# Kernel optimization log

Hardware: AMD Instinct MI355X
Metric: run time of the kernel (lower is better)

The kernel has to match this reference:

```python
import jax, jax.numpy as jnp
import numpy as np

MARGIN = 0.3


def setup_inputs() -> dict:
    key = jax.random.key(0)
    k1, k2 = jax.random.split(key)
    B, D, N_IDS = 8192, 256, 512
    emb = jax.random.normal(k1, (B, D), dtype=jnp.float32)
    emb = emb / jnp.linalg.norm(emb, axis=1, keepdims=True)  # L2-normalized as docstring states
    labels = jax.random.randint(k2, (B,), 0, N_IDS, dtype=jnp.int64)
    return {"embeddings": emb, "labels": labels}


def reference(embeddings, labels):
    B = embeddings.shape[0]
    # pairwise Euclidean distance via cosine similarity (embeddings are L2-normalized)
    sim = jnp.matmul(embeddings, embeddings.T)              # (B, B)
    dist = jnp.sqrt(jnp.clip(2.0 - 2.0 * sim, 0.0) + 1e-12)
    same = labels[:, None] == labels[None, :]               # (B, B)
    eye = jnp.eye(B, dtype=bool)
    pos_mask = same & ~eye
    neg_mask = ~same
    neg_inf = jnp.asarray(-jnp.inf, dist.dtype)
    pos_inf = jnp.asarray(jnp.inf, dist.dtype)
    dist_ap = jnp.max(jnp.where(pos_mask, dist, neg_inf), axis=1)  # hardest positive per anchor
    dist_an = jnp.min(jnp.where(neg_mask, dist, pos_inf), axis=1)  # hardest negative per anchor
    valid = jnp.any(pos_mask, axis=1) & jnp.any(neg_mask, axis=1)
    # MarginRankingLoss(dist_an, dist_ap, y=1) = mean(relu(dist_ap - dist_an + margin)) over valid anchors
    per = jnp.maximum(dist_ap - dist_an + MARGIN, 0.0)
    per = jnp.where(valid, per, 0.0)
    n_valid = jnp.sum(valid.astype(dist.dtype))
    loss = jnp.where(n_valid > 0, jnp.sum(per) / jnp.maximum(n_valid, 1.0), 0.0)
    return loss
```

## Files before the change

### kernel.cpp

```cpp
#include <hip/hip_runtime.h>
#include <hip/hip_bf16.h>


#define BDIM 8192
#define DDIM 256

typedef short bf16x8 __attribute__((ext_vector_type(8)));
typedef float f32x4  __attribute__((ext_vector_type(4)));
typedef unsigned short u16;

static __device__ __forceinline__ bf16x8 ld_frag(const u16* p) {
    return *reinterpret_cast<const bf16x8*>(p);
}

static __device__ __forceinline__ u16 f2bf(float f) {
    union { float f; unsigned int u; } x; x.f = f;
    unsigned int u = x.u;
    unsigned int r = u + 0x7fffu + ((u >> 16) & 1u);
    return (u16)(r >> 16);
}

static __device__ __forceinline__ void gload_lds16(const u16* g, u16* l) {
    __builtin_amdgcn_global_load_lds(
        (const __attribute__((address_space(1))) unsigned int*)g,
        (__attribute__((address_space(3))) unsigned int*)l, 16, 0, 0);
}

__global__ __launch_bounds__(256) void cvt_init_kernel(const float* __restrict__ in,
                                                       u16* __restrict__ out,
                                                       int* __restrict__ minpos,
                                                       int* __restrict__ maxneg) {
    int i = blockIdx.x * 256 + threadIdx.x;
    const float4 v = reinterpret_cast<const float4*>(in)[i];
    ushort4 o;
    o.x = f2bf(v.x); o.y = f2bf(v.y); o.z = f2bf(v.z); o.w = f2bf(v.w);
    reinterpret_cast<ushort4*>(out)[i] = o;
    if (i < BDIM) {
        minpos[i] = 0x7f800000;
        maxneg[i] = 0;
    }
}

__global__ __launch_bounds__(256, 2) void triplet_main(const u16* __restrict__ Ebf,
                                                       const int* __restrict__ labels,
                                                       int* __restrict__ minpos,
                                                       int* __restrict__ maxneg) {
    __shared__ __align__(16) u16 smem[3][32 * DDIM];
    __shared__ int slab[256];
    __shared__ int colmin[256], colmax[256];

    const int tid  = threadIdx.x;
    const int w    = tid >> 6;
    const int l    = tid & 63;
    const int quad = l >> 4;
    const int r16  = l & 15;

    int t = blockIdx.x, bi = 0;
    while (t >= 32 - bi) { t -= 32 - bi; ++bi; }
    const int bu = bi + t;

    const int mblk  = bi * 256 + w * 64;
    const int nbase = bu * 256;

    slab[tid]   = labels[nbase + tid];
    colmin[tid] = 0x7f800000;
    colmax[tid] = 0;

    bf16x8 a[4][8];
#pragma unroll
    for (int ms = 0; ms < 4; ++ms) {
        const u16* ap = Ebf + (size_t)(mblk + ms * 16 + r16) * DDIM + quad * 8;
#pragma unroll
        for (int k = 0; k < 8; ++k) a[ms][k] = ld_frag(ap + k * 32);
    }

    int lab_row[4][4];
#pragma unroll
    for (int ms = 0; ms < 4; ++ms)
#pragma unroll
        for (int r = 0; r < 4; ++r)
            lab_row[ms][r] = labels[mblk + ms * 16 + quad * 4 + r];

    float minp[4][4], maxn[4][4];
#pragma unroll
    for (int ms = 0; ms < 4; ++ms)
#pragma unroll
        for (int r = 0; r < 4; ++r) { minp[ms][r] = __builtin_inff(); maxn[ms][r] = -__builtin_inff(); }

    const int qs = quad ^ (r16 & 3);
    const int s4 = (r16 >> 2) & 1;

    auto stage = [&](int tt, int buf) {
        const int n1 = nbase + tt * 32;
#pragma unroll
        for (int it = 0; it < 4; ++it) {
            const int q = it * 256 + tid;
            const int r = q >> 5;
            const int c = (q & 31) ^ (r & 7);
            gload_lds16(Ebf + ((size_t)(n1 + r) << 8) + c * 8,
                        &smem[buf][0] + it * 2048 + w * 512);
        }
    };

    stage(0, 0);
    stage(1, 1);

    int cur = 0;
#pragma unroll 1
    for (int nn = 0; nn < 8; ++nn) {
        if (nn < 7) asm volatile("s_waitcnt vmcnt(4) lgkmcnt(0)" ::: "memory");
        else        asm volatile("s_waitcnt vmcnt(0) lgkmcnt(0)" ::: "memory");
        __builtin_amdgcn_s_barrier();
        __builtin_amdgcn_sched_barrier(0);

        if (nn + 2 < 8) {
            const int stg = (cur >= 1) ? cur - 1 : 2;
            stage(nn + 2, stg);
        }

        const int n0 = nbase + nn * 32;

        if (n0 + 32 > mblk) {
            int lab_c[2];
            lab_c[0] = slab[nn * 32 + r16];
            lab_c[1] = slab[nn * 32 + 16 + r16];

            f32x4 acc[4][2];
#pragma unroll
            for (int ms = 0; ms < 4; ++ms)
#pragma unroll
                for (int nt = 0; nt < 2; ++nt)
                    acc[ms][nt] = (f32x4){0.f, 0.f, 0.f, 0.f};

            const u16* bb = &smem[cur][0];
            const u16* bnt[2];
#pragma unroll
            for (int nt = 0; nt < 2; ++nt)
                bnt[nt] = bb + (nt * 16 + r16) * DDIM + qs * 8;

            __builtin_amdgcn_s_setprio(1);
#pragma unroll
            for (int k = 0; k < 8; ++k) {
                const int koff = ((k ^ s4) << 5);
                bf16x8 b[2];
#pragma unroll
                for (int nt = 0; nt < 2; ++nt) b[nt] = ld_frag(bnt[nt] + koff);
#pragma unroll
                for (int ms = 0; ms < 4; ++ms)
#pragma unroll
                    for (int nt = 0; nt < 2; ++nt)
                        acc[ms][nt] = __builtin_amdgcn_mfma_f32_16x16x32_bf16(
                            a[ms][k], b[nt], acc[ms][nt], 0, 0, 0);
            }
            __builtin_amdgcn_s_setprio(0);

            float cmin[2], cmax[2];
#pragma unroll
            for (int nt = 0; nt < 2; ++nt) { cmin[nt] = __builtin_inff(); cmax[nt] = -__builtin_inff(); }

            const bool diagTile = (n0 < mblk + 64) && (mblk < n0 + 32);
            if (__builtin_expect(diagTile, 0)) {
#pragma unroll
                for (int nt = 0; nt < 2; ++nt) {
                    const int colg = n0 + nt * 16 + r16;
#pragma unroll
                    for (int ms = 0; ms < 4; ++ms)
#pragma unroll
                        for (int r = 0; r < 4; ++r) {
                            const int rowg = mblk + ms * 16 + quad * 4 + r;
                            const float s = acc[ms][nt][r];
                            const bool same = (lab_c[nt] == lab_row[ms][r]);
                            const bool pos  = same && (colg != rowg);
                            const float pv = pos  ?  s : __builtin_inff();
                            const float nv = same ? -__builtin_inff() : s;
                            minp[ms][r] = fminf(minp[ms][r], pv);
                            maxn[ms][r] = fmaxf(maxn[ms][r], nv);
                            cmin[nt] = fminf(cmin[nt], pv);
                            cmax[nt] = fmaxf(cmax[nt], nv);
                        }
                }
            } else {
#pragma unroll
                for (int nt = 0; nt < 2; ++nt)
#pragma unroll
                    for (int ms = 0; ms < 4; ++ms)
#pragma unroll
                        for (int r = 0; r < 4; ++r) {
                            const float s = acc[ms][nt][r];
                            const bool same = (lab_c[nt] == lab_row[ms][r]);
                            const float pv = same ?  s : __builtin_inff();
                            const float nv = same ? -__builtin_inff() : s;
                            minp[ms][r] = fminf(minp[ms][r], pv);
                            maxn[ms][r] = fmaxf(maxn[ms][r], nv);
                            cmin[nt] = fminf(cmin[nt], pv);
                            cmax[nt] = fmaxf(cmax[nt], nv);
                        }
            }

#pragma unroll
            for (int mask = 16; mask <= 32; mask <<= 1) {
#pragma unroll
                for (int nt = 0; nt < 2; ++nt) {
                    cmin[nt] = fminf(cmin[nt], __shfl_xor(cmin[nt], mask, 64));
                    cmax[nt] = fmaxf(cmax[nt], __shfl_xor(cmax[nt], mask, 64));
                }
            }
            if (quad == 0) {
#pragma unroll
                for (int nt = 0; nt < 2; ++nt) {
                    const int cl = nn * 32 + nt * 16 + r16;
                    atomicMin(&colmin[cl], __float_as_int(cmin[nt] + 2.0f));
                    atomicMax(&colmax[cl], __float_as_int(cmax[nt] + 2.0f));
                }
            }
        }

        cur = (cur == 2) ? 0 : cur + 1;
    }

#pragma unroll
    for (int mask = 1; mask <= 8; mask <<= 1) {
#pragma unroll
        for (int ms = 0; ms < 4; ++ms)
#pragma unroll
            for (int r = 0; r < 4; ++r) {
                minp[ms][r] = fminf(minp[ms][r], __shfl_xor(minp[ms][r], mask, 64));
                maxn[ms][r] = fmaxf(maxn[ms][r], __shfl_xor(maxn[ms][r], mask, 64));
            }
    }
    if (r16 == 0) {
#pragma unroll
        for (int ms = 0; ms < 4; ++ms)
#pragma unroll
            for (int r = 0; r < 4; ++r) {
                const int rowg = mblk + ms * 16 + quad * 4 + r;
                atomicMin(minpos + rowg, __float_as_int(minp[ms][r] + 2.0f));
                atomicMax(maxneg + rowg, __float_as_int(maxn[ms][r] + 2.0f));
            }
    }

    __syncthreads();
    atomicMin(minpos + nbase + tid, colmin[tid]);
    atomicMax(maxneg + nbase + tid, colmax[tid]);
}

__global__ __launch_bounds__(1024) void finalize_kernel(const int* __restrict__ minpos,
                                                        const int* __restrict__ maxneg,
                                                        float* __restrict__ out) {
    __shared__ float ssum[16], scnt[16];
    float sum = 0.f, cnt = 0.f;
#pragma unroll
    for (int it = 0; it < 8; ++it) {
        const int i = it * 1024 + threadIdx.x;
        const float mp = __int_as_float(minpos[i]);
        const float mn = __int_as_float(maxneg[i]);
        if (mp < 1e30f && mn > 0.5f) {
            const float dap = sqrtf(fmaxf(6.0f - 2.0f * mp, 0.0f) + 1e-12f);
            const float dan = sqrtf(fmaxf(6.0f - 2.0f * mn, 0.0f) + 1e-12f);
            sum += fmaxf(dap - dan + 0.3f, 0.0f);
            cnt += 1.0f;
        }
    }
#pragma unroll
    for (int off = 32; off > 0; off >>= 1) {
        sum += __shfl_down(sum, off, 64);
        cnt += __shfl_down(cnt, off, 64);
    }
    const int wid = threadIdx.x >> 6;
    if ((threadIdx.x & 63) == 0) { ssum[wid] = sum; scnt[wid] = cnt; }
    __syncthreads();
    if (threadIdx.x == 0) {
        float S = 0.f, C = 0.f;
#pragma unroll
        for (int i = 0; i < 16; ++i) { S += ssum[i]; C += scnt[i]; }
        out[0] = (C > 0.f) ? (S / C) : 0.f;
    }
}

extern "C" void kernel_launch(void* const* d_in, const int* in_sizes, int n_in,
                              void* d_out, int out_size, void* d_ws, size_t ws_size,
                              hipStream_t stream) {
    const float* emb    = (const float*)d_in[0];
    const int*   labels = (const int*)d_in[1];
    float*       out    = (float*)d_out;

    u16* Ebf    = (u16*)d_ws;
    int* minpos = (int*)((char*)d_ws + (size_t)BDIM * DDIM * 2);
    int* maxneg = minpos + BDIM;

    cvt_init_kernel<<<dim3((BDIM * DDIM / 4) / 256), dim3(256), 0, stream>>>(emb, Ebf, minpos, maxneg);
    triplet_main<<<dim3(528), dim3(256), 0, stream>>>(Ebf, labels, minpos, maxneg);
    finalize_kernel<<<dim3(1), dim3(1024), 0, stream>>>(minpos, maxneg, out);
}
```

Measured before the change: 113.7 us.

## Split triangular tile work evenly across 512 blocks with tile-pair spanning

Replaces the one-block-per-256x256 tile-pair grid (528 blocks) with 512 blocks that each process a contiguous run of 8 or 9 sub-tiles (32-column slices) from the linearized pair list, possibly spanning two pairs. When a block crosses a pair boundary it flushes column and row reductions, reloads labels and A fragments, and continues the same pipelined loop. This is meant to cut the tail wave that 528 blocks leave on 256 CUs at 2 blocks per CU. The cost is extra flush, reload and barrier work at boundaries.

```diff
diff --git a/kernel.cpp b/kernel.cpp
--- a/kernel.cpp
+++ b/kernel.cpp
@@ -55,43 +55,86 @@
     const int quad = l >> 4;
     const int r16  = l & 15;
 
-    int t = blockIdx.x, bi = 0;
-    while (t >= 32 - bi) { t -= 32 - bi; ++bi; }
-    const int bu = bi + t;
-
-    const int mblk  = bi * 256 + w * 64;
-    const int nbase = bu * 256;
-
-    slab[tid]   = labels[nbase + tid];
+    const int blk   = blockIdx.x;
+    const int start = blk * 8 + (blk < 128 ? blk : 128);
+    const int count = (blk < 128) ? 9 : 8;
+    const int pF    = start >> 3;
+    const int pL    = (start + count - 1) >> 3;
+
+    int biF, buF, biL, buL;
+    {
+        int t = pF, b = 0;
+        while (t >= 32 - b) { t -= 32 - b; ++b; }
+        biF = b; buF = b + t;
+    }
+    {
+        int t = pL, b = 0;
+        while (t >= 32 - b) { t -= 32 - b; ++b; }
+        biL = b; buL = b + t;
+    }
+
+    slab[tid]   = labels[buF * 256 + tid];
     colmin[tid] = 0x7f800000;
     colmax[tid] = 0;
 
     bf16x8 a[4][8];
-#pragma unroll
-    for (int ms = 0; ms < 4; ++ms) {
-        const u16* ap = Ebf + (size_t)(mblk + ms * 16 + r16) * DDIM + quad * 8;
-#pragma unroll
-        for (int k = 0; k < 8; ++k) a[ms][k] = ld_frag(ap + k * 32);
-    }
-
     int lab_row[4][4];
-#pragma unroll
-    for (int ms = 0; ms < 4; ++ms)
-#pragma unroll
-        for (int r = 0; r < 4; ++r)
-            lab_row[ms][r] = labels[mblk + ms * 16 + quad * 4 + r];
+    auto loadA = [&](int bi) {
+        const int mb = bi * 256 + w * 64;
+#pragma unroll
+        for (int ms = 0; ms < 4; ++ms) {
+            const u16* ap = Ebf + (size_t)(mb + ms * 16 + r16) * DDIM + quad * 8;
+#pragma unroll
+            for (int k = 0; k < 8; ++k) a[ms][k] = ld_frag(ap + k * 32);
+        }
+#pragma unroll
+        for (int ms = 0; ms < 4; ++ms)
+#pragma unroll
+            for (int r = 0; r < 4; ++r)
+                lab_row[ms][r] = labels[mb + ms * 16 + quad * 4 + r];
+    };
+    loadA(biF);
 
     float minp[4][4], maxn[4][4];
-#pragma unroll
-    for (int ms = 0; ms < 4; ++ms)
-#pragma unroll
-        for (int r = 0; r < 4; ++r) { minp[ms][r] = __builtin_inff(); maxn[ms][r] = -__builtin_inff(); }
+    auto resetRC = [&]() {
+#pragma unroll
+        for (int ms = 0; ms < 4; ++ms)
+#pragma unroll
+            for (int r = 0; r < 4; ++r) { minp[ms][r] = __builtin_inff(); maxn[ms][r] = -__builtin_inff(); }
+    };
+    resetRC();
+
+    auto flushRows = [&](int bi) {
+        const int mb = bi * 256 + w * 64;
+#pragma unroll
+        for (int mask = 1; mask <= 8; mask <<= 1) {
+#pragma unroll
+            for (int ms = 0; ms < 4; ++ms)
+#pragma unroll
+                for (int r = 0; r < 4; ++r) {
+                    minp[ms][r] = fminf(minp[ms][r], __shfl_xor(minp[ms][r], mask, 64));
+                    maxn[ms][r] = fmaxf(maxn[ms][r], __shfl_xor(maxn[ms][r], mask, 64));
+                }
+        }
+        if (r16 == 0) {
+#pragma unroll
+            for (int ms = 0; ms < 4; ++ms)
+#pragma unroll
+                for (int r = 0; r < 4; ++r) {
+                    const int rowg = mb + ms * 16 + quad * 4 + r;
+                    atomicMin(minpos + rowg, __float_as_int(minp[ms][r] + 2.0f));
+                    atomicMax(maxneg + rowg, __float_as_int(maxn[ms][r] + 2.0f));
+                }
+        }
+    };
 
     const int qs = quad ^ (r16 & 3);
     const int s4 = (r16 >> 2) & 1;
 
-    auto stage = [&](int tt, int buf) {
-        const int n1 = nbase + tt * 32;
+    auto stage = [&](int s, int buf) {
+        const int T  = start + s;
+        const int bu = ((T >> 3) == pF) ? buF : buL;
+        const int n1 = bu * 256 + (T & 7) * 32;
 #pragma unroll
         for (int it = 0; it < 4; ++it) {
             const int q = it * 256 + tid;
@@ -106,19 +149,46 @@
     stage(1, 1);
 
     int cur = 0;
+    int curPair = pF;
 #pragma unroll 1
-    for (int nn = 0; nn < 8; ++nn) {
-        if (nn < 7) asm volatile("s_waitcnt vmcnt(4) lgkmcnt(0)" ::: "memory");
-        else        asm volatile("s_waitcnt vmcnt(0) lgkmcnt(0)" ::: "memory");
+    for (int s = 0; s < count; ++s) {
+        const int T  = start + s;
+        const int p  = T >> 3;
+        const int nn = T & 7;
+
+        if (s + 1 < count) asm volatile("s_waitcnt vmcnt(4) lgkmcnt(0)" ::: "memory");
+        else               asm volatile("s_waitcnt vmcnt(0) lgkmcnt(0)" ::: "memory");
         __builtin_amdgcn_s_barrier();
         __builtin_amdgcn_sched_barrier(0);
 
-        if (nn + 2 < 8) {
+        if (p != curPair) {
+            if (buL != buF) {
+                atomicMin(minpos + buF * 256 + tid, colmin[tid]);
+                atomicMax(maxneg + buF * 256 + tid, colmax[tid]);
+                colmin[tid] = 0x7f800000;
+                colmax[tid] = 0;
+                slab[tid] = labels[buL * 256 + tid];
+            }
+            if (biL != biF) {
+                flushRows(biF);
+                resetRC();
+                loadA(biL);
+            }
+            asm volatile("s_waitcnt lgkmcnt(0)" ::: "memory");
+            __builtin_amdgcn_s_barrier();
+            __builtin_amdgcn_sched_barrier(0);
+            curPair = p;
+        }
+
+        if (s + 2 < count) {
             const int stg = (cur >= 1) ? cur - 1 : 2;
-            stage(nn + 2, stg);
-        }
-
-        const int n0 = nbase + nn * 32;
+            stage(s + 2, stg);
+        }
+
+        const int bi   = (p == pF) ? biF : biL;
+        const int bu   = (p == pF) ? buF : buL;
+        const int mblk = bi * 256 + w * 64;
+        const int n0   = bu * 256 + nn * 32;
 
         if (n0 + 32 > mblk) {
             int lab_c[2];
@@ -168,11 +238,11 @@
 #pragma unroll
                         for (int r = 0; r < 4; ++r) {
                             const int rowg = mblk + ms * 16 + quad * 4 + r;
-                            const float s = acc[ms][nt][r];
+                            const float s2 = acc[ms][nt][r];
                             const bool same = (lab_c[nt] == lab_row[ms][r]);
                             const bool pos  = same && (colg != rowg);
-                            const float pv = pos  ?  s : __builtin_inff();
-                            const float nv = same ? -__builtin_inff() : s;
+                            const float pv = pos  ?  s2 : __builtin_inff();
+                            const float nv = same ? -__builtin_inff() : s2;
                             minp[ms][r] = fminf(minp[ms][r], pv);
                             maxn[ms][r] = fmaxf(maxn[ms][r], nv);
                             cmin[nt] = fminf(cmin[nt], pv);
@@ -186,10 +256,10 @@
                     for (int ms = 0; ms < 4; ++ms)
 #pragma unroll
                         for (int r = 0; r < 4; ++r) {
-                            const float s = acc[ms][nt][r];
+                            const float s2 = acc[ms][nt][r];
                             const bool same = (lab_c[nt] == lab_row[ms][r]);
-                            const float pv = same ?  s : __builtin_inff();
-                            const float nv = same ? -__builtin_inff() : s;
+                            const float pv = same ?  s2 : __builtin_inff();
+                            const float nv = same ? -__builtin_inff() : s2;
                             minp[ms][r] = fminf(minp[ms][r], pv);
                             maxn[ms][r] = fmaxf(maxn[ms][r], nv);
                             cmin[nt] = fminf(cmin[nt], pv);
@@ -218,30 +288,10 @@
         cur = (cur == 2) ? 0 : cur + 1;
     }
 
-#pragma unroll
-    for (int mask = 1; mask <= 8; mask <<= 1) {
-#pragma unroll
-        for (int ms = 0; ms < 4; ++ms)
-#pragma unroll
-            for (int r = 0; r < 4; ++r) {
-                minp[ms][r] = fminf(minp[ms][r], __shfl_xor(minp[ms][r], mask, 64));
-                maxn[ms][r] = fmaxf(maxn[ms][r], __shfl_xor(maxn[ms][r], mask, 64));
-            }
-    }
-    if (r16 == 0) {
-#pragma unroll
-        for (int ms = 0; ms < 4; ++ms)
-#pragma unroll
-            for (int r = 0; r < 4; ++r) {
-                const int rowg = mblk + ms * 16 + quad * 4 + r;
-                atomicMin(minpos + rowg, __float_as_int(minp[ms][r] + 2.0f));
-                atomicMax(maxneg + rowg, __float_as_int(maxn[ms][r] + 2.0f));
-            }
-    }
-
+    flushRows(biL);
     __syncthreads();
-    atomicMin(minpos + nbase + tid, colmin[tid]);
-    atomicMax(maxneg + nbase + tid, colmax[tid]);
+    atomicMin(minpos + buL * 256 + tid, colmin[tid]);
+    atomicMax(maxneg + buL * 256 + tid, colmax[tid]);
 }
 
 __global__ __launch_bounds__(1024) void finalize_kernel(const int* __restrict__ minpos,
@@ -289,6 +339,6 @@
     int* maxneg = minpos + BDIM;
 
     cvt_init_kernel<<<dim3((BDIM * DDIM / 4) / 256), dim3(256), 0, stream>>>(emb, Ebf, minpos, maxneg);
-    triplet_main<<<dim3(528), dim3(256), 0, stream>>>(Ebf, labels, minpos, maxneg);
+    triplet_main<<<dim3(512), dim3(256), 0, stream>>>(Ebf, labels, minpos, maxneg);
     finalize_kernel<<<dim3(1), dim3(1024), 0, stream>>>(minpos, maxneg, out);
 }
```

Result: faster. 110.5 us (-2.8%).
